# Kernel optimization log

Measured on AMD Instinct MI355X. Metric: run time of the kernel, lower is better.

Reference implementation:

```python
import jax, jax.numpy as jnp
import numpy as np

B = 8192
D_S, D_W, D_P, D_E, D_C, D_Z = 1024, 1024, 512, 1024, 512, 512
H_P = 2 * D_P          # particle hidden_dim default
RANK = D_W // 4        # low-rank A factor
EPS = 1e-5             # torch LayerNorm default eps


def _ln(x, g, b):
    m = jnp.mean(x, axis=-1, keepdims=True)
    v = jnp.var(x, axis=-1, keepdims=True)
    return (x - m) * jax.lax.rsqrt(v + EPS) * g + b


def setup_inputs() -> dict:
    key = jax.random.key(0)
    ks = iter(jax.random.split(key, 48))
    def randn(shape, scale=1.0):
        return jax.random.normal(next(ks), shape, dtype=jnp.float32) * scale
    def lin(dout, din):  # torch Linear: W [out,in], b [out]
        s = 1.0 / np.sqrt(din)
        return randn((dout, din), s), randn((dout,), s)
    inp = {}
    inp["s_prev"] = randn((B, D_S))
    inp["w_prev"] = randn((B, D_W))
    inp["p_prev"] = randn((B, D_P))
    inp["e_t"] = randn((B, D_E))
    inp["c_t"] = randn((B, D_C))
    d_in = D_S + D_E + D_C
    # fusion_net: Linear -> LN -> ReLU -> Linear
    inp["fw1"], inp["fb1"] = lin(2 * D_Z, d_in)
    inp["fln_g"] = jnp.ones((2 * D_Z,), jnp.float32)
    inp["fln_b"] = jnp.zeros((2 * D_Z,), jnp.float32)
    inp["fw2"], inp["fb2"] = lin(D_Z, 2 * D_Z)
    # wave subsystem
    inp["A_diag"] = jnp.zeros((D_W,), jnp.float32)
    inp["A_U"] = randn((D_W, RANK), 0.01)
    inp["A_V"] = randn((D_W, RANK), 0.01)
    inp["amod_w"], inp["amod_b"] = lin(D_W, D_C)
    inp["bnet_w"], inp["bnet_b"] = lin(D_W, D_C + D_Z)
    # particle subsystem phi
    inp["pw1"], inp["pb1"] = lin(H_P, D_P + D_Z + D_C)
    inp["pln_g"] = jnp.ones((H_P,), jnp.float32)
    inp["pln_b"] = jnp.zeros((H_P,), jnp.float32)
    inp["pw2"], inp["pb2"] = lin(H_P // 2, H_P)
    inp["pw3"], inp["pb3"] = lin(D_P, H_P // 2)
    # gate + mixing projections + output norm
    inp["gw"], inp["gb"] = lin(D_S, d_in)
    inp["uw"] = randn((D_S, D_W), 1.0 / np.sqrt(D_W))
    inp["up"] = randn((D_S, D_P), 1.0 / np.sqrt(D_P))
    inp["oln_g"] = jnp.ones((D_S,), jnp.float32)
    inp["oln_b"] = jnp.zeros((D_S,), jnp.float32)
    return inp


def reference(s_prev, w_prev, p_prev, e_t, c_t,
              fw1, fb1, fln_g, fln_b, fw2, fb2,
              A_diag, A_U, A_V, amod_w, amod_b, bnet_w, bnet_b,
              pw1, pb1, pln_g, pln_b, pw2, pb2, pw3, pb3,
              gw, gb, uw, up, oln_g, oln_b):
    # fusion: z_t = Linear(ReLU(LN(Linear([s||e||c]))))
    fin = jnp.concatenate([s_prev, e_t, c_t], axis=-1)      # [B, d_s+d_e+d_c]
    h = jax.nn.relu(_ln(fin @ fw1.T + fb1, fln_g, fln_b))
    z_t = h @ fw2.T + fb2                                   # [B, d_z]
    # wave: A = (diag(tanh(A_diag)*0.9) + A_U A_V^T) * mod[None,:]
    # so (A w)[b,i] = sum_j A_base[i,j] * (mod*w)[b,j] -> (mod*w) @ A_base^T
    A_base = jnp.diag(jnp.tanh(A_diag) * 0.9) + A_U @ A_V.T  # [d_w, d_w]
    mod = jnp.tanh(c_t @ amod_w.T + amod_b)                  # [B, d_w]
    w_linear = (mod * w_prev) @ A_base.T
    b_in = jnp.concatenate([c_t, z_t], axis=-1)
    w_t = w_linear + b_in @ bnet_w.T + bnet_b                # [B, d_w]
    # particle: p_t = p_prev + tanh(MLP([p||z||c]))
    pin = jnp.concatenate([p_prev, z_t, c_t], axis=-1)
    h1 = jax.nn.relu(_ln(pin @ pw1.T + pb1, pln_g, pln_b))
    h2 = jax.nn.relu(h1 @ pw2.T + pb2)
    p_t = p_prev + jnp.tanh(h2 @ pw3.T + pb3)                # [B, d_p]
    # gated mixing
    g_t = jax.nn.sigmoid(fin @ gw.T + gb)                    # [B, d_s]
    s_t = s_prev + g_t * (p_t @ up.T) + (1.0 - g_t) * (w_t @ uw.T)
    s_t = _ln(s_t, oln_g, oln_b)
    return (s_t, w_t, p_t)
```

## Files before the change

kernel.cpp:

```cpp
#include <hip/hip_runtime.h>
#include <math.h>

typedef unsigned short u16;
typedef __attribute__((ext_vector_type(8))) short short8;
typedef __attribute__((ext_vector_type(4))) float f32x4;

#define AS1C(p) ((const __attribute__((address_space(1))) void*)(p))
#define AS3(p)  ((__attribute__((address_space(3))) void*)(p))

static __device__ __forceinline__ float b2f(u16 h) {
    union { unsigned u; float f; } c; c.u = ((unsigned)h) << 16; return c.f;
}
static __device__ __forceinline__ u16 f2b(float f) {
    union { float f; unsigned u; } c; c.f = f;
    unsigned r = c.u + 0x7FFFu + ((c.u >> 16) & 1u);
    return (u16)(r >> 16);
}

#define EP_NONE     0
#define EP_RELU     1
#define EP_SIGMOID  2
#define EP_TANH_MUL 3
#define EP_TANH_ADD 4
#define EP_DIAG     5

template<int EP, bool BOTH>
__global__ __launch_bounds__(256)
void gemm_bt(const u16* __restrict__ A, int lda, const u16* __restrict__ W,
             const float* __restrict__ bias, const float* __restrict__ auxf,
             u16* __restrict__ outb, int ldd, float* __restrict__ outf,
             int M, int N, int K)
{
    __shared__ __align__(16) u16 As[128 * 64];
    __shared__ __align__(16) u16 Bs[128 * 64];

    const int tid  = threadIdx.x;
    const int nbm  = M >> 7;
    const int bm   = (int)blockIdx.x % nbm;
    const int bn   = (int)blockIdx.x / nbm;
    const int lane = tid & 63;
    const int wave = tid >> 6;
    const int wr   = wave >> 1;
    const int wc   = wave & 1;

    const int srow = tid >> 3;
    const int scol = (tid & 7) * 8;

    const u16* Ab = A + (size_t)(bm * 128 + srow) * lda + scol;
    const u16* Wb = W + (size_t)(bn * 128 + srow) * K + scol;
    u16* Asl = As + srow * 64 + scol;
    u16* Bsl = Bs + srow * 64 + scol;

    f32x4 acc[4][4];
#pragma unroll
    for (int m = 0; m < 4; ++m)
#pragma unroll
        for (int n = 0; n < 4; ++n) acc[m][n] = (f32x4){0.f, 0.f, 0.f, 0.f};

    const u16* ArdBase = As + ((wr * 64) + (lane & 15)) * 64 + (lane >> 4) * 8;
    const u16* BrdBase = Bs + ((wc * 64) + (lane & 15)) * 64 + (lane >> 4) * 8;

    for (int k0 = 0; k0 < K; k0 += 64) {
#pragma unroll
        for (int i = 0; i < 4; ++i) {
            __builtin_amdgcn_global_load_lds(AS1C(Ab + (size_t)(i * 32) * lda + k0),
                                             AS3(Asl + i * 32 * 64), 16, 0, 0);
            __builtin_amdgcn_global_load_lds(AS1C(Wb + (size_t)(i * 32) * K + k0),
                                             AS3(Bsl + i * 32 * 64), 16, 0, 0);
        }
        __syncthreads();
#pragma unroll
        for (int kk = 0; kk < 64; kk += 32) {
            short8 a[4], b[4];
#pragma unroll
            for (int m = 0; m < 4; ++m) a[m] = *(const short8*)(ArdBase + m * 16 * 64 + kk);
#pragma unroll
            for (int n = 0; n < 4; ++n) b[n] = *(const short8*)(BrdBase + n * 16 * 64 + kk);
#pragma unroll
            for (int m = 0; m < 4; ++m)
#pragma unroll
                for (int n = 0; n < 4; ++n)
                    acc[m][n] = __builtin_amdgcn_mfma_f32_16x16x32_bf16(a[m], b[n], acc[m][n], 0, 0, 0);
        }
        __syncthreads();
    }

    const int rbase = bm * 128 + wr * 64 + (lane >> 4) * 4;
    const int cbase = bn * 128 + wc * 64 + (lane & 15);
#pragma unroll
    for (int n = 0; n < 4; ++n) {
        const int C = cbase + n * 16;
        const float bv = bias ? bias[C] : 0.f;
#pragma unroll
        for (int m = 0; m < 4; ++m) {
            const int R0 = rbase + m * 16;
#pragma unroll
            for (int j = 0; j < 4; ++j) {
                const int R = R0 + j;
                float v = acc[m][n][j] + bv;
                if constexpr (EP == EP_RELU)          v = fmaxf(v, 0.f);
                else if constexpr (EP == EP_SIGMOID)  v = 1.f / (1.f + expf(-v));
                else if constexpr (EP == EP_TANH_MUL) v = tanhf(v) * auxf[(size_t)R * N + C];
                else if constexpr (EP == EP_TANH_ADD) v = auxf[(size_t)R * N + C] + tanhf(v);
                else if constexpr (EP == EP_DIAG)     { if (R == C) v += 0.9f * tanhf(auxf[R]); }
                outb[(size_t)R * ldd + C] = f2b(v);
                if constexpr (BOTH) outf[(size_t)R * N + C] = v;
            }
        }
    }
}

template<bool RELU>
__global__ __launch_bounds__(256)
void ln1024(u16* __restrict__ X, const float* __restrict__ gam, const float* __restrict__ bet)
{
    const int row = blockIdx.x;
    u16* xp = X + (size_t)row * 1024 + threadIdx.x * 4;
    u16 loc[4];
    *(uint2*)loc = *(const uint2*)xp;
    float x0 = b2f(loc[0]), x1 = b2f(loc[1]), x2 = b2f(loc[2]), x3 = b2f(loc[3]);
    float s = x0 + x1 + x2 + x3;
    float q = x0 * x0 + x1 * x1 + x2 * x2 + x3 * x3;
#pragma unroll
    for (int off = 32; off; off >>= 1) { s += __shfl_xor(s, off); q += __shfl_xor(q, off); }
    __shared__ float sm[8];
    const int wave = threadIdx.x >> 6, lane = threadIdx.x & 63;
    if (lane == 0) { sm[wave] = s; sm[4 + wave] = q; }
    __syncthreads();
    s = sm[0] + sm[1] + sm[2] + sm[3];
    q = sm[4] + sm[5] + sm[6] + sm[7];
    const float mean = s * (1.f / 1024.f);
    const float var  = q * (1.f / 1024.f) - mean * mean;
    const float inv  = rsqrtf(var + 1e-5f);
    const int cb = threadIdx.x * 4;
#pragma unroll
    for (int j = 0; j < 4; ++j) {
        float y = (b2f(loc[j]) - mean) * inv * gam[cb + j] + bet[cb + j];
        if (RELU) y = fmaxf(y, 0.f);
        loc[j] = f2b(y);
    }
    *(uint2*)xp = *(uint2*)loc;
}

__global__ __launch_bounds__(256)
void mix_ln(const float* __restrict__ sp, const u16* __restrict__ gt,
            const u16* __restrict__ pm, const u16* __restrict__ wm,
            const float* __restrict__ og, const float* __restrict__ ob,
            float* __restrict__ out)
{
    const int row = blockIdx.x;
    const size_t base = (size_t)row * 1024 + threadIdx.x * 4;
    float4 lsp = *(const float4*)(sp + base);
    u16 lg[4], lp[4], lw[4];
    *(uint2*)lg = *(const uint2*)(gt + base);
    *(uint2*)lp = *(const uint2*)(pm + base);
    *(uint2*)lw = *(const uint2*)(wm + base);
    float x[4];
    const float* lspp = (const float*)&lsp;
#pragma unroll
    for (int j = 0; j < 4; ++j) {
        float g = b2f(lg[j]);
        x[j] = lspp[j] + g * b2f(lp[j]) + (1.f - g) * b2f(lw[j]);
    }
    float s = x[0] + x[1] + x[2] + x[3];
    float q = x[0]*x[0] + x[1]*x[1] + x[2]*x[2] + x[3]*x[3];
#pragma unroll
    for (int off = 32; off; off >>= 1) { s += __shfl_xor(s, off); q += __shfl_xor(q, off); }
    __shared__ float sm[8];
    const int wave = threadIdx.x >> 6, lane = threadIdx.x & 63;
    if (lane == 0) { sm[wave] = s; sm[4 + wave] = q; }
    __syncthreads();
    s = sm[0] + sm[1] + sm[2] + sm[3];
    q = sm[4] + sm[5] + sm[6] + sm[7];
    const float mean = s * (1.f / 1024.f);
    const float var  = q * (1.f / 1024.f) - mean * mean;
    const float inv  = rsqrtf(var + 1e-5f);
    const int cb = threadIdx.x * 4;
    float4 o;
    float* op = (float*)&o;
#pragma unroll
    for (int j = 0; j < 4; ++j)
        op[j] = (x[j] - mean) * inv * og[cb + j] + ob[cb + j];
    *(float4*)(out + base) = o;
}

__global__ __launch_bounds__(256)
void cvt_f32_b16(const float* __restrict__ src, u16* __restrict__ dst, int n8)
{
    const int idx = blockIdx.x * 256 + threadIdx.x;
    if (idx >= n8) return;
    const float4 a = *(const float4*)(src + (size_t)idx * 8);
    const float4 b = *(const float4*)(src + (size_t)idx * 8 + 4);
    u16 o[8];
    const float* ap = (const float*)&a;
    const float* bp = (const float*)&b;
#pragma unroll
    for (int j = 0; j < 4; ++j) { o[j] = f2b(ap[j]); o[4 + j] = f2b(bp[j]); }
    *(uint4*)(dst + (size_t)idx * 8) = *(uint4*)o;
}

__global__ __launch_bounds__(256)
void ccopy_f32(const float* __restrict__ src, u16* __restrict__ dst,
               int srcCols8, int dstStride, int dstOff)
{
    const int idx = blockIdx.x * 256 + threadIdx.x;
    const int r = idx / srcCols8;
    const int c = idx % srcCols8;
    const float4 a = *(const float4*)(src + ((size_t)r * srcCols8 + c) * 8);
    const float4 b = *(const float4*)(src + ((size_t)r * srcCols8 + c) * 8 + 4);
    u16 o[8];
    const float* ap = (const float*)&a;
    const float* bp = (const float*)&b;
#pragma unroll
    for (int j = 0; j < 4; ++j) { o[j] = f2b(ap[j]); o[4 + j] = f2b(bp[j]); }
    *(uint4*)(dst + (size_t)r * dstStride + dstOff + (size_t)c * 8) = *(uint4*)o;
}

__global__ __launch_bounds__(256)
void ccopy_b16(const u16* __restrict__ src, u16* __restrict__ dst,
               int srcCols8, int dstStride, int dstOff)
{
    const int idx = blockIdx.x * 256 + threadIdx.x;
    const int r = idx / srcCols8;
    const int c = idx % srcCols8;
    const uint4 v = *(const uint4*)(src + ((size_t)r * srcCols8 + c) * 8);
    *(uint4*)(dst + (size_t)r * dstStride + dstOff + (size_t)c * 8) = v;
}

extern "C" void kernel_launch(void* const* d_in, const int* in_sizes, int n_in,
                              void* d_out, int out_size, void* d_ws, size_t ws_size,
                              hipStream_t stream)
{
    const float* s_prev = (const float*)d_in[0];
    const float* w_prev = (const float*)d_in[1];
    const float* p_prev = (const float*)d_in[2];
    const float* e_t    = (const float*)d_in[3];
    const float* c_t    = (const float*)d_in[4];
    const float* fw1    = (const float*)d_in[5];
    const float* fb1    = (const float*)d_in[6];
    const float* fln_g  = (const float*)d_in[7];
    const float* fln_b  = (const float*)d_in[8];
    const float* fw2    = (const float*)d_in[9];
    const float* fb2    = (const float*)d_in[10];
    const float* A_diag = (const float*)d_in[11];
    const float* A_U    = (const float*)d_in[12];
    const float* A_V    = (const float*)d_in[13];
    const float* amod_w = (const float*)d_in[14];
    const float* amod_b = (const float*)d_in[15];
    const float* bnet_w = (const float*)d_in[16];
    const float* bnet_b = (const float*)d_in[17];
    const float* pw1    = (const float*)d_in[18];
    const float* pb1    = (const float*)d_in[19];
    const float* pln_g  = (const float*)d_in[20];
    const float* pln_b  = (const float*)d_in[21];
    const float* pw2    = (const float*)d_in[22];
    const float* pb2    = (const float*)d_in[23];
    const float* pw3    = (const float*)d_in[24];
    const float* pb3    = (const float*)d_in[25];
    const float* gw     = (const float*)d_in[26];
    const float* gb     = (const float*)d_in[27];
    const float* uw     = (const float*)d_in[28];
    const float* up     = (const float*)d_in[29];
    const float* oln_g  = (const float*)d_in[30];
    const float* oln_b  = (const float*)d_in[31];

    float* out_s = (float*)d_out;
    float* out_w = out_s + (size_t)8192 * 1024;
    float* out_p = out_w + (size_t)8192 * 1024;

    u16* ws = (u16*)d_ws;
    u16* FIN  = ws;
    u16* W_bf = ws + 12582912;
    u16* H    = ws + 20971520;
    u16* P_bf = H;
    u16* Z    = ws + 29360128;
    u16* G    = ws + 33554432;
    u16* ACAT = ws + 41943040;
    u16* PM   = ACAT;
    u16* WM   = ACAT + 8388608;
    u16* WCAT = ws + 58720256;
    u16* wb   = ws + 60817408;
    u16* fw1b  = wb;
    u16* gwb   = wb + 2621440;
    u16* fw2b  = wb + 5242880;
    u16* amodb = wb + 5767168;
    u16* pw1b  = wb + 6291456;
    u16* pw2b  = wb + 7864320;
    u16* pw3b  = wb + 8388608;
    u16* uwb   = wb + 8650752;
    u16* upb   = wb + 9699328;
    u16* AUb   = wb + 10223616;
    u16* AVb   = wb + 10485760;

    const dim3 blk(256);
    auto cg = [](int n8) { return dim3((unsigned)((n8 + 255) / 256)); };
    auto g128 = [](int M, int N) { return dim3((unsigned)((M / 128) * (N / 128))); };

    cvt_f32_b16<<<cg(327680), blk, 0, stream>>>(fw1, fw1b, 327680);
    cvt_f32_b16<<<cg(327680), blk, 0, stream>>>(gw, gwb, 327680);
    cvt_f32_b16<<<cg(65536), blk, 0, stream>>>(fw2, fw2b, 65536);
    cvt_f32_b16<<<cg(65536), blk, 0, stream>>>(amod_w, amodb, 65536);
    cvt_f32_b16<<<cg(196608), blk, 0, stream>>>(pw1, pw1b, 196608);
    cvt_f32_b16<<<cg(65536), blk, 0, stream>>>(pw2, pw2b, 65536);
    cvt_f32_b16<<<cg(32768), blk, 0, stream>>>(pw3, pw3b, 32768);
    cvt_f32_b16<<<cg(131072), blk, 0, stream>>>(uw, uwb, 131072);
    cvt_f32_b16<<<cg(65536), blk, 0, stream>>>(up, upb, 65536);
    cvt_f32_b16<<<cg(32768), blk, 0, stream>>>(A_U, AUb, 32768);
    cvt_f32_b16<<<cg(32768), blk, 0, stream>>>(A_V, AVb, 32768);

    ccopy_f32<<<4096, blk, 0, stream>>>(s_prev, FIN, 128, 2560, 0);
    ccopy_f32<<<4096, blk, 0, stream>>>(e_t,    FIN, 128, 2560, 1024);
    ccopy_f32<<<2048, blk, 0, stream>>>(c_t,    FIN, 64,  2560, 2048);

    gemm_bt<EP_NONE, false><<<g128(8192, 1024), blk, 0, stream>>>(
        FIN, 2560, fw1b, fb1, nullptr, H, 1024, nullptr, 8192, 1024, 2560);
    ln1024<true><<<8192, blk, 0, stream>>>(H, fln_g, fln_b);
    gemm_bt<EP_NONE, false><<<g128(8192, 512), blk, 0, stream>>>(
        H, 1024, fw2b, fb2, nullptr, Z, 512, nullptr, 8192, 512, 1024);

    gemm_bt<EP_SIGMOID, false><<<g128(8192, 1024), blk, 0, stream>>>(
        FIN, 2560, gwb, gb, nullptr, G, 1024, nullptr, 8192, 1024, 2560);

    gemm_bt<EP_TANH_MUL, false><<<g128(8192, 1024), blk, 0, stream>>>(
        FIN + 2048, 2560, amodb, amod_b, w_prev, ACAT, 2048, nullptr, 8192, 1024, 512);
    gemm_bt<EP_DIAG, false><<<g128(1024, 1024), blk, 0, stream>>>(
        AUb, 256, AVb, nullptr, A_diag, WCAT, 2048, nullptr, 1024, 1024, 256);
    ccopy_f32<<<2048, blk, 0, stream>>>(c_t, ACAT, 64, 2048, 1024);
    ccopy_b16<<<2048, blk, 0, stream>>>(Z,   ACAT, 64, 2048, 1536);
    ccopy_f32<<<512, blk, 0, stream>>>(bnet_w, WCAT, 128, 2048, 1024);
    gemm_bt<EP_NONE, true><<<g128(8192, 1024), blk, 0, stream>>>(
        ACAT, 2048, WCAT, bnet_b, nullptr, W_bf, 1024, out_w, 8192, 1024, 2048);

    ccopy_f32<<<2048, blk, 0, stream>>>(p_prev, FIN, 64, 1536, 0);
    ccopy_b16<<<2048, blk, 0, stream>>>(Z,      FIN, 64, 1536, 512);
    ccopy_f32<<<2048, blk, 0, stream>>>(c_t,    FIN, 64, 1536, 1024);
    gemm_bt<EP_NONE, false><<<g128(8192, 1024), blk, 0, stream>>>(
        FIN, 1536, pw1b, pb1, nullptr, H, 1024, nullptr, 8192, 1024, 1536);
    ln1024<true><<<8192, blk, 0, stream>>>(H, pln_g, pln_b);
    gemm_bt<EP_RELU, false><<<g128(8192, 512), blk, 0, stream>>>(
        H, 1024, pw2b, pb2, nullptr, Z, 512, nullptr, 8192, 512, 1024);
    gemm_bt<EP_TANH_ADD, true><<<g128(8192, 512), blk, 0, stream>>>(
        Z, 512, pw3b, pb3, p_prev, P_bf, 512, out_p, 8192, 512, 512);

    gemm_bt<EP_NONE, false><<<g128(8192, 1024), blk, 0, stream>>>(
        P_bf, 512, upb, nullptr, nullptr, PM, 1024, nullptr, 8192, 1024, 512);
    gemm_bt<EP_NONE, false><<<g128(8192, 1024), blk, 0, stream>>>(
        W_bf, 1024, uwb, nullptr, nullptr, WM, 1024, nullptr, 8192, 1024, 1024);
    mix_ln<<<8192, blk, 0, stream>>>(s_prev, G, PM, WM, oln_g, oln_b, out_s);
}
```

Before: 554.9 us.

## Batch independent GEMMs into grouped launches and merge copy kernels

Replaces the templated per-GEMM kernel with a grouped GEMM kernel that takes up to three descriptors and picks one per block, so independent GEMMs (fusion fw1 with gate, fw2 with amod and the A build, bnet with pw1, pw2 with uw) share a single launch. All weight conversions and concat copies are merged into two descriptor-driven copy kernels. The aim is fewer launches and better GPU fill for small grids. In exchange the epilogue branches at runtime instead of being specialized at compile time, which may cost some registers or instructions.

```diff
diff --git a/kernel.cpp b/kernel.cpp
--- a/kernel.cpp
+++ b/kernel.cpp
@@ -24,20 +24,31 @@
 #define EP_TANH_ADD 4
 #define EP_DIAG     5
 
-template<int EP, bool BOTH>
+struct GDesc {
+    const u16* A;
+    const u16* W;
+    const float* bias;
+    const float* auxf;
+    u16* outb;
+    float* outf;
+    int lda, ldd, N, K, ep, nbm;
+};
+
+struct GArgs { GDesc d0, d1, d2; int s1, s2; };
+
 __global__ __launch_bounds__(256)
-void gemm_bt(const u16* __restrict__ A, int lda, const u16* __restrict__ W,
-             const float* __restrict__ bias, const float* __restrict__ auxf,
-             u16* __restrict__ outb, int ldd, float* __restrict__ outf,
-             int M, int N, int K)
+void gemm_multi(GArgs ga)
 {
     __shared__ __align__(16) u16 As[128 * 64];
     __shared__ __align__(16) u16 Bs[128 * 64];
 
+    const int bid = (int)blockIdx.x;
+    GDesc dd = (bid < ga.s1) ? ga.d0 : ((bid < ga.s2) ? ga.d1 : ga.d2);
+    const int b = bid - ((bid < ga.s1) ? 0 : ((bid < ga.s2) ? ga.s1 : ga.s2));
+
     const int tid  = threadIdx.x;
-    const int nbm  = M >> 7;
-    const int bm   = (int)blockIdx.x % nbm;
-    const int bn   = (int)blockIdx.x / nbm;
+    const int bm   = b % dd.nbm;
+    const int bn   = b / dd.nbm;
     const int lane = tid & 63;
     const int wave = tid >> 6;
     const int wr   = wave >> 1;
@@ -46,8 +57,10 @@
     const int srow = tid >> 3;
     const int scol = (tid & 7) * 8;
 
-    const u16* Ab = A + (size_t)(bm * 128 + srow) * lda + scol;
-    const u16* Wb = W + (size_t)(bn * 128 + srow) * K + scol;
+    const int lda = dd.lda, K = dd.K, N = dd.N, ldd = dd.ldd;
+
+    const u16* Ab = dd.A + (size_t)(bm * 128 + srow) * lda + scol;
+    const u16* Wb = dd.W + (size_t)(bn * 128 + srow) * K + scol;
     u16* Asl = As + srow * 64 + scol;
     u16* Bsl = Bs + srow * 64 + scol;
 
@@ -71,26 +84,27 @@
         __syncthreads();
 #pragma unroll
         for (int kk = 0; kk < 64; kk += 32) {
-            short8 a[4], b[4];
+            short8 a[4], bb[4];
 #pragma unroll
             for (int m = 0; m < 4; ++m) a[m] = *(const short8*)(ArdBase + m * 16 * 64 + kk);
 #pragma unroll
-            for (int n = 0; n < 4; ++n) b[n] = *(const short8*)(BrdBase + n * 16 * 64 + kk);
+            for (int n = 0; n < 4; ++n) bb[n] = *(const short8*)(BrdBase + n * 16 * 64 + kk);
 #pragma unroll
             for (int m = 0; m < 4; ++m)
 #pragma unroll
                 for (int n = 0; n < 4; ++n)
-                    acc[m][n] = __builtin_amdgcn_mfma_f32_16x16x32_bf16(a[m], b[n], acc[m][n], 0, 0, 0);
+                    acc[m][n] = __builtin_amdgcn_mfma_f32_16x16x32_bf16(a[m], bb[n], acc[m][n], 0, 0, 0);
         }
         __syncthreads();
     }
 
     const int rbase = bm * 128 + wr * 64 + (lane >> 4) * 4;
     const int cbase = bn * 128 + wc * 64 + (lane & 15);
+    const int ep = dd.ep;
 #pragma unroll
     for (int n = 0; n < 4; ++n) {
         const int C = cbase + n * 16;
-        const float bv = bias ? bias[C] : 0.f;
+        const float bv = dd.bias ? dd.bias[C] : 0.f;
 #pragma unroll
         for (int m = 0; m < 4; ++m) {
             const int R0 = rbase + m * 16;
@@ -98,13 +112,13 @@
             for (int j = 0; j < 4; ++j) {
                 const int R = R0 + j;
                 float v = acc[m][n][j] + bv;
-                if constexpr (EP == EP_RELU)          v = fmaxf(v, 0.f);
-                else if constexpr (EP == EP_SIGMOID)  v = 1.f / (1.f + expf(-v));
-                else if constexpr (EP == EP_TANH_MUL) v = tanhf(v) * auxf[(size_t)R * N + C];
-                else if constexpr (EP == EP_TANH_ADD) v = auxf[(size_t)R * N + C] + tanhf(v);
-                else if constexpr (EP == EP_DIAG)     { if (R == C) v += 0.9f * tanhf(auxf[R]); }
-                outb[(size_t)R * ldd + C] = f2b(v);
-                if constexpr (BOTH) outf[(size_t)R * N + C] = v;
+                if (ep == EP_RELU)          v = fmaxf(v, 0.f);
+                else if (ep == EP_SIGMOID)  v = 1.f / (1.f + expf(-v));
+                else if (ep == EP_TANH_MUL) v = tanhf(v) * dd.auxf[(size_t)R * N + C];
+                else if (ep == EP_TANH_ADD) v = dd.auxf[(size_t)R * N + C] + tanhf(v);
+                else if (ep == EP_DIAG)     { if (R == C) v += 0.9f * tanhf(dd.auxf[R]); }
+                dd.outb[(size_t)R * ldd + C] = f2b(v);
+                if (dd.outf) dd.outf[(size_t)R * N + C] = v;
             }
         }
     }
@@ -184,47 +198,33 @@
     *(float4*)(out + base) = o;
 }
 
+struct CDesc { const void* src; u16* dst; int srcCols8; int dstStride; int dstOff; unsigned end; int isbf16; };
+struct CArgs { CDesc d[16]; unsigned total; };
+
 __global__ __launch_bounds__(256)
-void cvt_f32_b16(const float* __restrict__ src, u16* __restrict__ dst, int n8)
-{
-    const int idx = blockIdx.x * 256 + threadIdx.x;
-    if (idx >= n8) return;
-    const float4 a = *(const float4*)(src + (size_t)idx * 8);
-    const float4 b = *(const float4*)(src + (size_t)idx * 8 + 4);
+void multi_copy(CArgs ca)
+{
+    const unsigned idx = blockIdx.x * 256 + threadIdx.x;
+    if (idx >= ca.total) return;
+    int i = 0; unsigned start = 0;
+    while (idx >= ca.d[i].end) { start = ca.d[i].end; ++i; }
+    const CDesc cd = ca.d[i];
+    const unsigned local = idx - start;
+    const int r = local / cd.srcCols8;
+    const int c = local % cd.srcCols8;
     u16 o[8];
-    const float* ap = (const float*)&a;
-    const float* bp = (const float*)&b;
-#pragma unroll
-    for (int j = 0; j < 4; ++j) { o[j] = f2b(ap[j]); o[4 + j] = f2b(bp[j]); }
-    *(uint4*)(dst + (size_t)idx * 8) = *(uint4*)o;
-}
-
-__global__ __launch_bounds__(256)
-void ccopy_f32(const float* __restrict__ src, u16* __restrict__ dst,
-               int srcCols8, int dstStride, int dstOff)
-{
-    const int idx = blockIdx.x * 256 + threadIdx.x;
-    const int r = idx / srcCols8;
-    const int c = idx % srcCols8;
-    const float4 a = *(const float4*)(src + ((size_t)r * srcCols8 + c) * 8);
-    const float4 b = *(const float4*)(src + ((size_t)r * srcCols8 + c) * 8 + 4);
-    u16 o[8];
-    const float* ap = (const float*)&a;
-    const float* bp = (const float*)&b;
-#pragma unroll
-    for (int j = 0; j < 4; ++j) { o[j] = f2b(ap[j]); o[4 + j] = f2b(bp[j]); }
-    *(uint4*)(dst + (size_t)r * dstStride + dstOff + (size_t)c * 8) = *(uint4*)o;
-}
-
-__global__ __launch_bounds__(256)
-void ccopy_b16(const u16* __restrict__ src, u16* __restrict__ dst,
-               int srcCols8, int dstStride, int dstOff)
-{
-    const int idx = blockIdx.x * 256 + threadIdx.x;
-    const int r = idx / srcCols8;
-    const int c = idx % srcCols8;
-    const uint4 v = *(const uint4*)(src + ((size_t)r * srcCols8 + c) * 8);
-    *(uint4*)(dst + (size_t)r * dstStride + dstOff + (size_t)c * 8) = v;
+    if (cd.isbf16) {
+        *(uint4*)o = *(const uint4*)((const u16*)cd.src + ((size_t)r * cd.srcCols8 + c) * 8);
+    } else {
+        const float* s = (const float*)cd.src + ((size_t)r * cd.srcCols8 + c) * 8;
+        const float4 a = *(const float4*)s;
+        const float4 bq = *(const float4*)(s + 4);
+        const float* ap = (const float*)&a;
+        const float* bp = (const float*)&bq;
+#pragma unroll
+        for (int j = 0; j < 4; ++j) { o[j] = f2b(ap[j]); o[4 + j] = f2b(bp[j]); }
+    }
+    *(uint4*)(cd.dst + (size_t)r * cd.dstStride + cd.dstOff + (size_t)c * 8) = *(uint4*)o;
 }
 
 extern "C" void kernel_launch(void* const* d_in, const int* in_sizes, int n_in,
@@ -293,58 +293,97 @@
     u16* AVb   = wb + 10485760;
 
     const dim3 blk(256);
-    auto cg = [](int n8) { return dim3((unsigned)((n8 + 255) / 256)); };
-    auto g128 = [](int M, int N) { return dim3((unsigned)((M / 128) * (N / 128))); };
-
-    cvt_f32_b16<<<cg(327680), blk, 0, stream>>>(fw1, fw1b, 327680);
-    cvt_f32_b16<<<cg(327680), blk, 0, stream>>>(gw, gwb, 327680);
-    cvt_f32_b16<<<cg(65536), blk, 0, stream>>>(fw2, fw2b, 65536);
-    cvt_f32_b16<<<cg(65536), blk, 0, stream>>>(amod_w, amodb, 65536);
-    cvt_f32_b16<<<cg(196608), blk, 0, stream>>>(pw1, pw1b, 196608);
-    cvt_f32_b16<<<cg(65536), blk, 0, stream>>>(pw2, pw2b, 65536);
-    cvt_f32_b16<<<cg(32768), blk, 0, stream>>>(pw3, pw3b, 32768);
-    cvt_f32_b16<<<cg(131072), blk, 0, stream>>>(uw, uwb, 131072);
-    cvt_f32_b16<<<cg(65536), blk, 0, stream>>>(up, upb, 65536);
-    cvt_f32_b16<<<cg(32768), blk, 0, stream>>>(A_U, AUb, 32768);
-    cvt_f32_b16<<<cg(32768), blk, 0, stream>>>(A_V, AVb, 32768);
-
-    ccopy_f32<<<4096, blk, 0, stream>>>(s_prev, FIN, 128, 2560, 0);
-    ccopy_f32<<<4096, blk, 0, stream>>>(e_t,    FIN, 128, 2560, 1024);
-    ccopy_f32<<<2048, blk, 0, stream>>>(c_t,    FIN, 64,  2560, 2048);
-
-    gemm_bt<EP_NONE, false><<<g128(8192, 1024), blk, 0, stream>>>(
-        FIN, 2560, fw1b, fb1, nullptr, H, 1024, nullptr, 8192, 1024, 2560);
+
+    {
+        CArgs ca; unsigned cum = 0; int nd = 0;
+        auto push = [&](const void* src, u16* dst, int cols8, int stride, int off,
+                        int rows, int isbf) {
+            cum += (unsigned)rows * cols8;
+            ca.d[nd++] = CDesc{src, dst, cols8, stride, off, cum, isbf};
+        };
+        push(fw1,    fw1b,  320, 2560, 0,    1024, 0);
+        push(gw,     gwb,   320, 2560, 0,    1024, 0);
+        push(fw2,    fw2b,  128, 1024, 0,    512,  0);
+        push(amod_w, amodb, 64,  512,  0,    1024, 0);
+        push(pw1,    pw1b,  192, 1536, 0,    1024, 0);
+        push(pw2,    pw2b,  128, 1024, 0,    512,  0);
+        push(pw3,    pw3b,  64,  512,  0,    512,  0);
+        push(uw,     uwb,   128, 1024, 0,    1024, 0);
+        push(up,     upb,   64,  512,  0,    1024, 0);
+        push(A_U,    AUb,   32,  256,  0,    1024, 0);
+        push(A_V,    AVb,   32,  256,  0,    1024, 0);
+        push(s_prev, FIN,   128, 2560, 0,    8192, 0);
+        push(e_t,    FIN,   128, 2560, 1024, 8192, 0);
+        push(c_t,    FIN,   64,  2560, 2048, 8192, 0);
+        push(c_t,    ACAT,  64,  2048, 1024, 8192, 0);
+        push(bnet_w, WCAT,  128, 2048, 1024, 1024, 0);
+        ca.total = cum;
+        multi_copy<<<dim3((cum + 255) / 256), blk, 0, stream>>>(ca);
+    }
+
+    {
+        GArgs ga;
+        ga.d0 = GDesc{FIN, fw1b, fb1, nullptr, H, nullptr, 2560, 1024, 1024, 2560, EP_NONE,    64};
+        ga.d1 = GDesc{FIN, gwb,  gb,  nullptr, G, nullptr, 2560, 1024, 1024, 2560, EP_SIGMOID, 64};
+        ga.d2 = ga.d1; ga.s1 = 512; ga.s2 = 1024;
+        gemm_multi<<<dim3(1024), blk, 0, stream>>>(ga);
+    }
     ln1024<true><<<8192, blk, 0, stream>>>(H, fln_g, fln_b);
-    gemm_bt<EP_NONE, false><<<g128(8192, 512), blk, 0, stream>>>(
-        H, 1024, fw2b, fb2, nullptr, Z, 512, nullptr, 8192, 512, 1024);
-
-    gemm_bt<EP_SIGMOID, false><<<g128(8192, 1024), blk, 0, stream>>>(
-        FIN, 2560, gwb, gb, nullptr, G, 1024, nullptr, 8192, 1024, 2560);
-
-    gemm_bt<EP_TANH_MUL, false><<<g128(8192, 1024), blk, 0, stream>>>(
-        FIN + 2048, 2560, amodb, amod_b, w_prev, ACAT, 2048, nullptr, 8192, 1024, 512);
-    gemm_bt<EP_DIAG, false><<<g128(1024, 1024), blk, 0, stream>>>(
-        AUb, 256, AVb, nullptr, A_diag, WCAT, 2048, nullptr, 1024, 1024, 256);
-    ccopy_f32<<<2048, blk, 0, stream>>>(c_t, ACAT, 64, 2048, 1024);
-    ccopy_b16<<<2048, blk, 0, stream>>>(Z,   ACAT, 64, 2048, 1536);
-    ccopy_f32<<<512, blk, 0, stream>>>(bnet_w, WCAT, 128, 2048, 1024);
-    gemm_bt<EP_NONE, true><<<g128(8192, 1024), blk, 0, stream>>>(
-        ACAT, 2048, WCAT, bnet_b, nullptr, W_bf, 1024, out_w, 8192, 1024, 2048);
-
-    ccopy_f32<<<2048, blk, 0, stream>>>(p_prev, FIN, 64, 1536, 0);
-    ccopy_b16<<<2048, blk, 0, stream>>>(Z,      FIN, 64, 1536, 512);
-    ccopy_f32<<<2048, blk, 0, stream>>>(c_t,    FIN, 64, 1536, 1024);
-    gemm_bt<EP_NONE, false><<<g128(8192, 1024), blk, 0, stream>>>(
-        FIN, 1536, pw1b, pb1, nullptr, H, 1024, nullptr, 8192, 1024, 1536);
+
+    {
+        GArgs ga;
+        ga.d0 = GDesc{H,          fw2b,  fb2,    nullptr, Z,    nullptr, 1024, 512,  512,  1024, EP_NONE,     64};
+        ga.d1 = GDesc{FIN + 2048, amodb, amod_b, w_prev,  ACAT, nullptr, 2560, 2048, 1024, 512,  EP_TANH_MUL, 64};
+        ga.d2 = GDesc{AUb,        AVb,   nullptr, A_diag, WCAT, nullptr, 256,  2048, 1024, 256,  EP_DIAG,     8};
+        ga.s1 = 256; ga.s2 = 768;
+        gemm_multi<<<dim3(832), blk, 0, stream>>>(ga);
+    }
+
+    {
+        CArgs ca; unsigned cum = 0; int nd = 0;
+        auto push = [&](const void* src, u16* dst, int cols8, int stride, int off,
+                        int rows, int isbf) {
+            cum += (unsigned)rows * cols8;
+            ca.d[nd++] = CDesc{src, dst, cols8, stride, off, cum, isbf};
+        };
+        push(p_prev, FIN,  64, 1536, 0,    8192, 0);
+        push(Z,      FIN,  64, 1536, 512,  8192, 1);
+        push(c_t,    FIN,  64, 1536, 1024, 8192, 0);
+        push(Z,      ACAT, 64, 2048, 1536, 8192, 1);
+        ca.total = cum;
+        multi_copy<<<dim3((cum + 255) / 256), blk, 0, stream>>>(ca);
+    }
+
+    {
+        GArgs ga;
+        ga.d0 = GDesc{ACAT, WCAT, bnet_b, nullptr, W_bf, out_w, 2048, 1024, 1024, 2048, EP_NONE, 64};
+        ga.d1 = GDesc{FIN,  pw1b, pb1,    nullptr, H,    nullptr, 1536, 1024, 1024, 1536, EP_NONE, 64};
+        ga.d2 = ga.d1; ga.s1 = 512; ga.s2 = 1024;
+        gemm_multi<<<dim3(1024), blk, 0, stream>>>(ga);
+    }
     ln1024<true><<<8192, blk, 0, stream>>>(H, pln_g, pln_b);
-    gemm_bt<EP_RELU, false><<<g128(8192, 512), blk, 0, stream>>>(
-        H, 1024, pw2b, pb2, nullptr, Z, 512, nullptr, 8192, 512, 1024);
-    gemm_bt<EP_TANH_ADD, true><<<g128(8192, 512), blk, 0, stream>>>(
-        Z, 512, pw3b, pb3, p_prev, P_bf, 512, out_p, 8192, 512, 512);
-
-    gemm_bt<EP_NONE, false><<<g128(8192, 1024), blk, 0, stream>>>(
-        P_bf, 512, upb, nullptr, nullptr, PM, 1024, nullptr, 8192, 1024, 512);
-    gemm_bt<EP_NONE, false><<<g128(8192, 1024), blk, 0, stream>>>(
-        W_bf, 1024, uwb, nullptr, nullptr, WM, 1024, nullptr, 8192, 1024, 1024);
+
+    {
+        GArgs ga;
+        ga.d0 = GDesc{H,    pw2b, pb2,    nullptr, Z,  nullptr, 1024, 512,  512,  1024, EP_RELU, 64};
+        ga.d1 = GDesc{W_bf, uwb,  nullptr, nullptr, WM, nullptr, 1024, 1024, 1024, 1024, EP_NONE, 64};
+        ga.d2 = ga.d1; ga.s1 = 256; ga.s2 = 768;
+        gemm_multi<<<dim3(768), blk, 0, stream>>>(ga);
+    }
+
+    {
+        GArgs ga;
+        ga.d0 = GDesc{Z, pw3b, pb3, p_prev, P_bf, out_p, 512, 512, 512, 512, EP_TANH_ADD, 64};
+        ga.d1 = ga.d0; ga.d2 = ga.d0; ga.s1 = 256; ga.s2 = 256;
+        gemm_multi<<<dim3(256), blk, 0, stream>>>(ga);
+    }
+
+    {
+        GArgs ga;
+        ga.d0 = GDesc{P_bf, upb, nullptr, nullptr, PM, nullptr, 512, 1024, 1024, 512, EP_NONE, 64};
+        ga.d1 = ga.d0; ga.d2 = ga.d0; ga.s1 = 512; ga.s2 = 512;
+        gemm_multi<<<dim3(512), blk, 0, stream>>>(ga);
+    }
+
     mix_ln<<<8192, blk, 0, stream>>>(s_prev, G, PM, WM, oln_g, oln_b, out_s);
 }
```

Result: faster. 534.7 us (-3.6%).
